# Performance work log

Hardware: AMD Instinct MI355X
Metric: run time of the kernel (lower is better)

The kernel has to match this reference:

```python
import jax, jax.numpy as jnp
import numpy as np

N_NODES = 100_000
N_FACES = 200_000
N_EDGES1 = 800_000
N_TRIP = 500_000
H = 64
GEO_IN = 10 + 2 * 23  # 56
N_INTER = 3
DEPTH = 3  # finaldepth; total SPNN layers = DEPTH + 1
PI = float(np.pi)
EPS = 1e-5


def setup_inputs() -> dict:
    key = jax.random.key(0)
    ks = jax.random.split(key, 12)
    s = 0.05
    input_feature = jax.random.normal(ks[0], (N_NODES, H), jnp.float32)
    coords = jax.random.normal(ks[1], (N_NODES, 3), jnp.float32)
    face_norm = jax.random.normal(ks[2], (N_FACES, 3), jnp.float32)
    face_x = jax.random.normal(ks[3], (N_FACES, 23), jnp.float32)
    edge_whichface = jax.random.randint(ks[4], (N_EDGES1,), 0, N_FACES)
    edge_index_2rd = jax.random.randint(ks[5], (3, N_TRIP), 0, N_NODES)
    edx_ij = jax.random.randint(ks[6], (N_TRIP,), 0, N_EDGES1)
    edx_rand = jax.random.randint(ks[7], (N_TRIP,), 0, N_EDGES1)
    edx_jk = jnp.where(jnp.arange(N_TRIP) % 2 == 0, edx_ij, edx_rand)
    att = jnp.ones((2,), jnp.float32)
    W_geo = jax.random.normal(ks[8], (H, GEO_IN), jnp.float32) * s
    b_geo = jnp.zeros((H,), jnp.float32)
    g_geo = jnp.ones((H,), jnp.float32)
    be_geo = jnp.zeros((H,), jnp.float32)
    spnn_W0 = jax.random.normal(ks[9], (N_INTER, 2, H, 4 * H), jnp.float32) * s
    spnn_b0 = jnp.zeros((N_INTER, 2, H), jnp.float32)
    spnn_Wr = jax.random.normal(ks[10], (N_INTER, 2, DEPTH, H, H), jnp.float32) * s
    spnn_br = jnp.zeros((N_INTER, 2, DEPTH, H), jnp.float32)
    bn_g = jnp.ones((N_INTER, 2, DEPTH + 1, H), jnp.float32)
    bn_b = jnp.zeros((N_INTER, 2, DEPTH + 1, H), jnp.float32)
    return dict(input_feature=input_feature, coords=coords, face_norm=face_norm,
                face_x=face_x, att=att, W_geo=W_geo, b_geo=b_geo, g_geo=g_geo,
                be_geo=be_geo, spnn_W0=spnn_W0, spnn_b0=spnn_b0, spnn_Wr=spnn_Wr,
                spnn_br=spnn_br, bn_g=bn_g, bn_b=bn_b,
                edge_whichface=edge_whichface, edge_index_2rd=edge_index_2rd,
                edx_jk=edx_jk, edx_ij=edx_ij)


def _bn(x, g, b):
    # BatchNorm1d, training mode (batch stats, biased variance)
    mean = x.mean(0)
    var = ((x - mean) ** 2).mean(0)
    return (x - mean) * jax.lax.rsqrt(var + EPS) * g + b


def _masked_bn(x, mf, g, b):
    # BatchNorm over only the masked rows (original code runs BN on x_i[mask]);
    # applied to all rows, masked rows selected afterward -> identical math.
    cnt = jnp.maximum(mf.sum(), 1.0)
    mean = (x * mf).sum(0) / cnt
    var = (((x - mean) ** 2) * mf).sum(0) / cnt
    return (x - mean) * jax.lax.rsqrt(var + EPS) * g + b


def _angle(v1, v2):
    c = jnp.cross(v1, v2)
    return jnp.arctan2(jnp.linalg.norm(c, axis=1), (v1 * v2).sum(1))


def reference(input_feature, coords, face_norm, face_x, att, W_geo, b_geo,
              g_geo, be_geo, spnn_W0, spnn_b0, spnn_Wr, spnn_br, bn_g, bn_b,
              edge_whichface, edge_index_2rd, edx_jk, edx_ij):
    i, j, k = edge_index_2rd
    f_ij = edge_whichface[edx_ij]
    f_jk = edge_whichface[edx_jk]
    # angle_face is computed then multiplied by 0 in the original
    angle_face = (PI - _angle(face_norm[f_ij], face_norm[f_jk])) * 0.0
    cj, ci, ck = coords[j], coords[i], coords[k]
    d_ij = jnp.linalg.norm(cj - ci, axis=1)
    d_jk = jnp.linalg.norm(cj - ck, axis=1)
    theta = _angle(cj - ci, ck - cj)
    same_face = f_ij == f_jk
    geo = jnp.concatenate([d_ij[:, None], d_jk[:, None], theta[:, None],
                           angle_face[:, None], cj, ci,
                           face_x[f_ij], face_x[f_jk]], axis=-1)  # [E, 56]
    geo = jax.nn.relu(_bn(geo @ W_geo.T + b_geo, g_geo, be_geo))  # [E, H]

    nf = input_feature
    masks = [same_face, ~same_face]
    outs = []
    for t in range(N_INTER):
        xcat = jnp.concatenate([nf[i], nf[j], nf[k], geo], axis=-1)  # [E, 4H]
        x_out = jnp.zeros((xcat.shape[0], H), xcat.dtype)
        for bi in range(2):
            mf = masks[bi].astype(xcat.dtype)[:, None]
            x = jax.nn.relu(_masked_bn(xcat @ spnn_W0[t, bi].T + spnn_b0[t, bi],
                                       mf, bn_g[t, bi, 0], bn_b[t, bi, 0]))
            for l in range(DEPTH):
                x = jax.nn.relu(_masked_bn(x @ spnn_Wr[t, bi, l].T + spnn_br[t, bi, l],
                                           mf, bn_g[t, bi, l + 1], bn_b[t, bi, l + 1]))
            x = jax.nn.leaky_relu(x) * att[bi]
            x_out = x_out + x * mf
        nf = jax.ops.segment_sum(x_out, i, num_segments=N_NODES)
        outs.append(nf)
    return jnp.stack(outs)  # [N_INTER, N, H] (list in original)
```

## Files before the change

kernel.cpp:

```cpp
#include <hip/hip_runtime.h>

#define E_TRIP 500000
#define EPAD   500224
#define NTILE64 (EPAD/64)
#define NBLK256 (EPAD/256)
#define NBLK    1954
#define NN 100000
#define NBIN (2*NN)
#define EPSF 1e-5f
#define RSTAT 64

typedef _Float16 f16;
typedef _Float16 f16x8 __attribute__((ext_vector_type(8)));
typedef float f32x4 __attribute__((ext_vector_type(4)));

__global__ __launch_bounds__(256) void k_count(const int* __restrict__ ewf,
    const int* __restrict__ exij, const int* __restrict__ exjk,
    unsigned char* __restrict__ biedge, int* __restrict__ cb0)
{
  __shared__ int wcnt[4];
  int e = blockIdx.x*256 + threadIdx.x;
  bool active = e < E_TRIP;
  int b = 0;
  if (active) {
    int fij = ewf[exij[e]];
    int fjk = ewf[exjk[e]];
    b = (fij == fjk) ? 0 : 1;
    biedge[e] = (unsigned char)b;
  }
  unsigned long long m0 = __ballot(active && b==0);
  int lane = threadIdx.x & 63, wv = threadIdx.x >> 6;
  if (lane == 0) wcnt[wv] = (int)__popcll(m0);
  __syncthreads();
  if (threadIdx.x == 0) cb0[blockIdx.x] = wcnt[0] + wcnt[1] + wcnt[2] + wcnt[3];
}

__global__ __launch_bounds__(1024) void k_scanb(const int* __restrict__ cb0, int* __restrict__ sc)
{
  __shared__ int s[2048];
  int tid = threadIdx.x;
  int i0 = tid, i1 = tid + 1024;
  s[i0] = (i0 < NBLK) ? cb0[i0] : 0;
  s[i1] = (i1 < NBLK) ? cb0[i1] : 0;
  __syncthreads();
  for (int off = 1; off < 2048; off <<= 1) {
    int v0 = (i0 >= off) ? s[i0 - off] : 0;
    int v1 = (i1 >= off) ? s[i1 - off] : 0;
    __syncthreads();
    s[i0] += v0; s[i1] += v1;
    __syncthreads();
  }
  if (tid == 0) {
    int c0 = s[NBLK-1];
    int c0p = (c0 + 63) & ~63;
    sc[4] = c0; sc[5] = c0p; sc[6] = E_TRIP - c0;
  }
}

__global__ __launch_bounds__(256) void k_cvt(const float* __restrict__ W0,
    const float* __restrict__ Wr, const float* __restrict__ nf,
    f16* __restrict__ W0h, f16* __restrict__ Wrh, f16* __restrict__ nfh)
{
  int i = (blockIdx.x*256 + threadIdx.x) * 4;
  if (i < 98304) {
    float4 v = *(const float4*)(W0 + i);
    W0h[i]=(f16)v.x; W0h[i+1]=(f16)v.y; W0h[i+2]=(f16)v.z; W0h[i+3]=(f16)v.w;
  } else if (i < 172032) {
    int j = i - 98304;
    float4 v = *(const float4*)(Wr + j);
    Wrh[j]=(f16)v.x; Wrh[j+1]=(f16)v.y; Wrh[j+2]=(f16)v.z; Wrh[j+3]=(f16)v.w;
  } else {
    int j = i - 172032;
    if (j < NN*64) {
      float4 v = *(const float4*)(nf + j);
      nfh[j]=(f16)v.x; nfh[j+1]=(f16)v.y; nfh[j+2]=(f16)v.z; nfh[j+3]=(f16)v.w;
    }
  }
}

__global__ __launch_bounds__(256) void k_hist(const unsigned char* __restrict__ biedge,
    const int* __restrict__ eidx, int* __restrict__ cnt)
{
  int e = blockIdx.x*256 + threadIdx.x;
  if (e < E_TRIP) {
    int key = (int)biedge[e]*NN + eidx[e];
    atomicAdd(&cnt[key], 1);
  }
}

__global__ __launch_bounds__(512) void k_scan1(const int* __restrict__ cnt,
    int* __restrict__ start, int* __restrict__ btot)
{
  __shared__ int s[512];
  int tid = threadIdx.x;
  int g = blockIdx.x*512 + tid;
  int x = (g < NBIN) ? cnt[g] : 0;
  s[tid] = x; __syncthreads();
  #pragma unroll
  for (int off = 1; off < 512; off <<= 1) {
    int v = (tid >= off) ? s[tid-off] : 0;
    __syncthreads();
    s[tid] += v;
    __syncthreads();
  }
  if (g < NBIN) start[g] = s[tid] - x;
  if (tid == 511) btot[blockIdx.x] = s[511];
}

__global__ __launch_bounds__(512) void k_scan2(int* __restrict__ btot)
{
  __shared__ int s[512];
  int tid = threadIdx.x;
  int x = (tid < 391) ? btot[tid] : 0;
  s[tid] = x; __syncthreads();
  #pragma unroll
  for (int off = 1; off < 512; off <<= 1) {
    int v = (tid >= off) ? s[tid-off] : 0;
    __syncthreads();
    s[tid] += v;
    __syncthreads();
  }
  if (tid < 391) btot[tid] = s[tid] - x;
}

__global__ __launch_bounds__(512) void k_scan3(int* __restrict__ start,
    int* __restrict__ cur, const int* __restrict__ btot, const int* __restrict__ sc)
{
  int tid = threadIdx.x;
  int g = blockIdx.x*512 + tid;
  if (g < NBIN) {
    int v = start[g] + btot[blockIdx.x];
    if (g >= NN) v += sc[5] - sc[4];
    start[g] = v;
    cur[g] = v;
  }
  if (g == 0) start[NBIN] = sc[5] + sc[6];
}

__global__ __launch_bounds__(256) void k_place(const unsigned char* __restrict__ biedge,
    const int* __restrict__ eidx, int* __restrict__ cur,
    int* __restrict__ epos, int* __restrict__ ip, int* __restrict__ jp, int* __restrict__ kp)
{
  int e = blockIdx.x*256 + threadIdx.x;
  if (e < E_TRIP) {
    int i = eidx[e];
    int key = (int)biedge[e]*NN + i;
    int pos = atomicAdd(&cur[key], 1);
    epos[pos] = e;
    ip[pos] = i;
    jp[pos] = eidx[E_TRIP + e];
    kp[pos] = eidx[2*E_TRIP + e];
  }
}

__global__ __launch_bounds__(256) void k_geo(
    const float* __restrict__ coords, const float* __restrict__ facex,
    const int* __restrict__ ewf, const int* __restrict__ exij, const int* __restrict__ exjk,
    const float* __restrict__ Wgeo, const float* __restrict__ bgeo,
    const int* __restrict__ sc, const int* __restrict__ epos,
    const int* __restrict__ ip, const int* __restrict__ jp, const int* __restrict__ kp,
    f16* __restrict__ zgeo, float* __restrict__ gstats)
{
  __shared__ f16 lds[256*72];
  __shared__ float sstat[64][2];
  int tid = threadIdx.x;
  int base = blockIdx.x*256;
  int c0 = sc[4], c0p = sc[5], c1 = sc[6];
  if (tid < 128) ((float*)sstat)[tid] = 0.f;
  {
    int p = base + tid;
    bool valid = (p < c0) || (p >= c0p && p < c0p + c1);
    f16* lrow = lds + tid*72;
    if (valid) {
      int e = epos[p];
      int ii = ip[p], jj = jp[p], kk = kp[p];
      float cix = coords[ii*3+0], ciy = coords[ii*3+1], ciz = coords[ii*3+2];
      float cjx = coords[jj*3+0], cjy = coords[jj*3+1], cjz = coords[jj*3+2];
      float ckx = coords[kk*3+0], cky = coords[kk*3+1], ckz = coords[kk*3+2];
      float v1x = cjx-cix, v1y = cjy-ciy, v1z = cjz-ciz;
      float v2x = ckx-cjx, v2y = cky-cjy, v2z = ckz-cjz;
      float dij = sqrtf(v1x*v1x + v1y*v1y + v1z*v1z);
      float djk = sqrtf(v2x*v2x + v2y*v2y + v2z*v2z);
      float cx = v1y*v2z - v1z*v2y;
      float cy = v1z*v2x - v1x*v2z;
      float cz = v1x*v2y - v1y*v2x;
      float theta = atan2f(sqrtf(cx*cx+cy*cy+cz*cz), v1x*v2x+v1y*v2y+v1z*v2z);
      lrow[0]=(f16)dij; lrow[1]=(f16)djk; lrow[2]=(f16)theta; lrow[3]=(f16)0.f;
      lrow[4]=(f16)cjx; lrow[5]=(f16)cjy; lrow[6]=(f16)cjz;
      lrow[7]=(f16)cix; lrow[8]=(f16)ciy; lrow[9]=(f16)ciz;
      int fij = ewf[exij[e]], fjk = ewf[exjk[e]];
      const float* fx1 = facex + (size_t)fij*23;
      const float* fx2 = facex + (size_t)fjk*23;
      for (int c = 0; c < 23; c++) lrow[10+c] = (f16)fx1[c];
      for (int c = 0; c < 23; c++) lrow[33+c] = (f16)fx2[c];
      for (int c = 56; c < 64; c++) lrow[c] = (f16)0.f;
    } else {
      for (int c = 0; c < 64; c++) lrow[c] = (f16)0.f;
    }
  }
  __syncthreads();
  int wv = tid>>6, lane = tid&63, lg = lane>>4, lr = lane&15;
  f16x8 Bf[4][2];
  #pragma unroll
  for (int nt = 0; nt < 4; nt++) {
    #pragma unroll
    for (int ks = 0; ks < 2; ks++) {
      int n = nt*16 + lr;
      int kb = ks*32 + lg*8;
      f16x8 w;
      if (kb < 56) {
        float4 w0 = *(const float4*)(Wgeo + n*56 + kb);
        float4 w1 = *(const float4*)(Wgeo + n*56 + kb + 4);
        w[0]=(f16)w0.x; w[1]=(f16)w0.y; w[2]=(f16)w0.z; w[3]=(f16)w0.w;
        w[4]=(f16)w1.x; w[5]=(f16)w1.y; w[6]=(f16)w1.z; w[7]=(f16)w1.w;
      } else {
        #pragma unroll
        for (int j2 = 0; j2 < 8; j2++) w[j2] = (f16)0.f;
      }
      Bf[nt][ks] = w;
    }
  }
  float ssum[4] = {0,0,0,0}, ssq[4] = {0,0,0,0};
  for (int mt = 0; mt < 4; mt++) {
    int rbase = wv*64 + mt*16;
    f16x8 A0 = *(const f16x8*)(lds + (rbase+lr)*72 + lg*8);
    f16x8 A1 = *(const f16x8*)(lds + (rbase+lr)*72 + 32 + lg*8);
    f32x4 acc[4];
    #pragma unroll
    for (int nt = 0; nt < 4; nt++) { acc[nt][0]=0.f; acc[nt][1]=0.f; acc[nt][2]=0.f; acc[nt][3]=0.f; }
    #pragma unroll
    for (int nt = 0; nt < 4; nt++) {
      acc[nt] = __builtin_amdgcn_mfma_f32_16x16x32_f16(A0, Bf[nt][0], acc[nt], 0, 0, 0);
      acc[nt] = __builtin_amdgcn_mfma_f32_16x16x32_f16(A1, Bf[nt][1], acc[nt], 0, 0, 0);
    }
    #pragma unroll
    for (int nt = 0; nt < 4; nt++) {
      int n = nt*16 + lr;
      float bg = bgeo[n];
      #pragma unroll
      for (int rg = 0; rg < 4; rg++) {
        int rloc = rbase + lg*4 + rg;
        int p = base + rloc;
        bool valid = (p < c0) || (p >= c0p && p < c0p + c1);
        float z = valid ? (acc[nt][rg] + bg) : 0.f;
        ssum[nt] += z; ssq[nt] += z*z;
        lds[rloc*72 + n] = (f16)z;
      }
    }
  }
  #pragma unroll
  for (int nt = 0; nt < 4; nt++) {
    float v = ssum[nt]; v += __shfl_xor(v, 16); v += __shfl_xor(v, 32);
    float w = ssq[nt];  w += __shfl_xor(w, 16); w += __shfl_xor(w, 32);
    if (lane < 16) { atomicAdd(&sstat[nt*16+lane][0], v); atomicAdd(&sstat[nt*16+lane][1], w); }
  }
  __syncthreads();
  {
    int p = base + tid;
    #pragma unroll
    for (int c = 0; c < 8; c++) {
      f16x8 v = *(const f16x8*)(lds + tid*72 + c*8);
      *(f16x8*)(zgeo + (size_t)p*64 + c*8) = v;
    }
  }
  if (tid < 128) {
    float v = ((float*)sstat)[tid];
    if (v != 0.f) atomicAdd(&gstats[(blockIdx.x & (RSTAT-1))*256 + tid], v);
  }
}

__global__ __launch_bounds__(256) void k_layer0(
    const f16* __restrict__ nfsrc, const f16* __restrict__ zgeo,
    const f16* __restrict__ W0p, const float* __restrict__ b0p,
    const float* __restrict__ g_geo, const float* __restrict__ be_geo,
    const float* __restrict__ geostats, float* __restrict__ outstats,
    const int* __restrict__ sc, const int* __restrict__ ip,
    const int* __restrict__ jp, const int* __restrict__ kp,
    f16* __restrict__ z0)
{
  __shared__ f16 lds[64*264];
  __shared__ float geoscale[64], geoshift[64];
  __shared__ float sstat[2][64][2];
  int tid = threadIdx.x;
  int c0 = sc[4], c0p = sc[5], c1 = sc[6];
  if (tid < 64) {
    float s = 0.f, sq = 0.f;
    #pragma unroll 8
    for (int r = 0; r < RSTAT; r++) {
      s  += geostats[r*256 + tid*2];
      sq += geostats[r*256 + tid*2 + 1];
    }
    float mean = s * (1.f/(float)E_TRIP);
    float var  = sq * (1.f/(float)E_TRIP) - mean*mean;
    float rstd = rsqrtf(var + EPSF);
    float scl = g_geo[tid]*rstd;
    geoscale[tid] = scl;
    geoshift[tid] = be_geo[tid] - mean*scl;
  }
  ((float*)sstat)[tid] = 0.f;
  __syncthreads();
  int wv = tid>>6, lane = tid&63, lg = lane>>4, lr = lane&15;
  float s0sum[4]={0,0,0,0}, s0sq[4]={0,0,0,0}, s1sum[4]={0,0,0,0}, s1sq[4]={0,0,0,0};
  for (int tile = blockIdx.x; tile < NTILE64; tile += gridDim.x) {
    int rowbase = tile*64;
    int branch = (rowbase >= c0p) ? 1 : 0;
    {
      int r = tid >> 2, q = tid & 3;
      int p = rowbase + r;
      bool valid = (p < c0) || (p >= c0p && p < c0p + c1);
      f16* rowp = lds + r*264 + q*64;
      if (q < 3) {
        if (valid) {
          int idx = (q==0 ? ip : (q==1 ? jp : kp))[p];
          const f16* src = nfsrc + (size_t)idx*64;
          #pragma unroll
          for (int c = 0; c < 8; c++) *(f16x8*)(rowp + c*8) = *(const f16x8*)(src + c*8);
        } else {
          f16x8 u;
          #pragma unroll
          for (int j2 = 0; j2 < 8; j2++) u[j2] = (f16)0.f;
          #pragma unroll
          for (int c = 0; c < 8; c++) *(f16x8*)(rowp + c*8) = u;
        }
      } else {
        if (valid) {
          const f16* zg = zgeo + (size_t)p*64;
          #pragma unroll
          for (int c = 0; c < 8; c++) {
            f16x8 raw = *(const f16x8*)(zg + c*8);
            f16x8 u;
            #pragma unroll
            for (int j2 = 0; j2 < 8; j2++) {
              int f = c*8 + j2;
              float x = fmaxf((float)raw[j2]*geoscale[f] + geoshift[f], 0.f);
              u[j2] = (f16)x;
            }
            *(f16x8*)(rowp + c*8) = u;
          }
        } else {
          f16x8 u;
          #pragma unroll
          for (int j2 = 0; j2 < 8; j2++) u[j2] = (f16)0.f;
          #pragma unroll
          for (int c = 0; c < 8; c++) *(f16x8*)(rowp + c*8) = u;
        }
      }
    }
    __syncthreads();
    {
      int r0 = wv*16;
      const f16* Wb = W0p + branch*16384;
      f32x4 acc[4];
      #pragma unroll
      for (int nt = 0; nt < 4; nt++) { acc[nt][0]=0.f; acc[nt][1]=0.f; acc[nt][2]=0.f; acc[nt][3]=0.f; }
      #pragma unroll
      for (int ks = 0; ks < 8; ks++) {
        f16x8 A = *(const f16x8*)(lds + (r0+lr)*264 + (ks*4+lg)*8);
        #pragma unroll
        for (int nt = 0; nt < 4; nt++) {
          f16x8 B = *(const f16x8*)(Wb + (nt*16+lr)*256 + ks*32 + lg*8);
          acc[nt] = __builtin_amdgcn_mfma_f32_16x16x32_f16(A, B, acc[nt], 0, 0, 0);
        }
      }
      #pragma unroll
      for (int nt = 0; nt < 4; nt++) {
        int n = nt*16 + lr;
        float bias = b0p[branch*64 + n];
        #pragma unroll
        for (int rg = 0; rg < 4; rg++) {
          int rloc = r0 + lg*4 + rg;
          int p = rowbase + rloc;
          bool valid = (p < c0) || (p >= c0p && p < c0p + c1);
          float z = valid ? (acc[nt][rg] + bias) : 0.f;
          if (branch == 0) { s0sum[nt] += z; s0sq[nt] += z*z; }
          else             { s1sum[nt] += z; s1sq[nt] += z*z; }
          lds[rloc*264 + n] = (f16)z;
        }
      }
    }
    __syncthreads();
    {
      int r = tid>>2, q = tid&3;
      int p = rowbase + r;
      f16x8 v0 = *(const f16x8*)(lds + r*264 + q*16);
      f16x8 v1 = *(const f16x8*)(lds + r*264 + q*16 + 8);
      *(f16x8*)(z0 + (size_t)p*64 + q*16) = v0;
      *(f16x8*)(z0 + (size_t)p*64 + q*16 + 8) = v1;
    }
    __syncthreads();
  }
  #pragma unroll
  for (int nt = 0; nt < 4; nt++) {
    float v, w;
    v = s0sum[nt]; v += __shfl_xor(v,16); v += __shfl_xor(v,32);
    w = s0sq[nt];  w += __shfl_xor(w,16); w += __shfl_xor(w,32);
    if (lane < 16) { atomicAdd(&sstat[0][nt*16+lane][0], v); atomicAdd(&sstat[0][nt*16+lane][1], w); }
    v = s1sum[nt]; v += __shfl_xor(v,16); v += __shfl_xor(v,32);
    w = s1sq[nt];  w += __shfl_xor(w,16); w += __shfl_xor(w,32);
    if (lane < 16) { atomicAdd(&sstat[1][nt*16+lane][0], v); atomicAdd(&sstat[1][nt*16+lane][1], w); }
  }
  __syncthreads();
  {
    float v = ((float*)sstat)[tid];
    if (v != 0.f) atomicAdd(&outstats[(blockIdx.x & (RSTAT-1))*256 + tid], v);
  }
}

__global__ __launch_bounds__(256) void k_hidden(
    const f16* __restrict__ zin, f16* __restrict__ zout,
    const f16* __restrict__ Wp, const float* __restrict__ biasp,
    const float* __restrict__ bngp, const float* __restrict__ bnbp,
    const float* __restrict__ instats, float* __restrict__ outstats,
    const int* __restrict__ sc)
{
  __shared__ float lscale[2][64], lshift[2][64];
  __shared__ float sstat[2][64][2];
  __shared__ f16 ldso[4][16*72];
  int tid = threadIdx.x;
  int c0 = sc[4], c0p = sc[5], c1 = sc[6];
  if (tid < 128) {
    int b = tid>>6, n = tid&63;
    int cb = b ? c1 : c0; if (cb < 1) cb = 1;
    float inv = 1.f/(float)cb;
    int idx = (b*64+n)*2;
    float s = 0.f, sq = 0.f;
    #pragma unroll 8
    for (int r = 0; r < RSTAT; r++) {
      s  += instats[r*256 + idx];
      sq += instats[r*256 + idx + 1];
    }
    float mean = s*inv, var = sq*inv - mean*mean;
    float rstd = rsqrtf(var + EPSF);
    float scl = bngp[b*256+n]*rstd;
    lscale[b][n] = scl;
    lshift[b][n] = bnbp[b*256+n] - mean*scl;
  }
  ((float*)sstat)[tid] = 0.f;
  __syncthreads();
  int wv = tid>>6, lane = tid&63, lg = lane>>4, lr = lane&15;
  f16* myldso = ldso[wv];
  float s0sum[4]={0,0,0,0}, s0sq[4]={0,0,0,0}, s1sum[4]={0,0,0,0}, s1sq[4]={0,0,0,0};
  for (int tile = blockIdx.x; tile < NTILE64; tile += gridDim.x) {
    int rowbase = tile*64;
    int branch = (rowbase >= c0p) ? 1 : 0;
    int rgl = rowbase + wv*16 + lr;
    f16x8 Af[2];
    #pragma unroll
    for (int ks = 0; ks < 2; ks++) {
      f16x8 raw = *(const f16x8*)(zin + (size_t)rgl*64 + ks*32 + lg*8);
      f16x8 A;
      #pragma unroll
      for (int j2 = 0; j2 < 8; j2++) {
        int f = ks*32 + lg*8 + j2;
        float x = fmaxf((float)raw[j2]*lscale[branch][f] + lshift[branch][f], 0.f);
        A[j2] = (f16)x;
      }
      Af[ks] = A;
    }
    f32x4 acc[4];
    #pragma unroll
    for (int nt = 0; nt < 4; nt++) { acc[nt][0]=0.f; acc[nt][1]=0.f; acc[nt][2]=0.f; acc[nt][3]=0.f; }
    #pragma unroll
    for (int ks = 0; ks < 2; ks++) {
      #pragma unroll
      for (int nt = 0; nt < 4; nt++) {
        f16x8 B = *(const f16x8*)(Wp + branch*12288 + (nt*16+lr)*64 + ks*32 + lg*8);
        acc[nt] = __builtin_amdgcn_mfma_f32_16x16x32_f16(Af[ks], B, acc[nt], 0, 0, 0);
      }
    }
    #pragma unroll
    for (int nt = 0; nt < 4; nt++) {
      int n = nt*16 + lr;
      float bias = biasp[branch*192 + n];
      #pragma unroll
      for (int rg = 0; rg < 4; rg++) {
        int rloc = lg*4 + rg;
        int p = rowbase + wv*16 + rloc;
        bool valid = (p < c0) || (p >= c0p && p < c0p + c1);
        float z = valid ? (acc[nt][rg] + bias) : 0.f;
        if (branch == 0) { s0sum[nt] += z; s0sq[nt] += z*z; }
        else             { s1sum[nt] += z; s1sq[nt] += z*z; }
        myldso[rloc*72 + n] = (f16)z;
      }
    }
    {
      int r2 = lane>>2, q = lane&3;
      int p2 = rowbase + wv*16 + r2;
      f16x8 v0 = *(const f16x8*)(myldso + r2*72 + q*8);
      f16x8 v1 = *(const f16x8*)(myldso + r2*72 + 32 + q*8);
      *(f16x8*)(zout + (size_t)p2*64 + q*8) = v0;
      *(f16x8*)(zout + (size_t)p2*64 + 32 + q*8) = v1;
    }
  }
  #pragma unroll
  for (int nt = 0; nt < 4; nt++) {
    float v, w;
    v = s0sum[nt]; v += __shfl_xor(v,16); v += __shfl_xor(v,32);
    w = s0sq[nt];  w += __shfl_xor(w,16); w += __shfl_xor(w,32);
    if (lane < 16) { atomicAdd(&sstat[0][nt*16+lane][0], v); atomicAdd(&sstat[0][nt*16+lane][1], w); }
    v = s1sum[nt]; v += __shfl_xor(v,16); v += __shfl_xor(v,32);
    w = s1sq[nt];  w += __shfl_xor(w,16); w += __shfl_xor(w,32);
    if (lane < 16) { atomicAdd(&sstat[1][nt*16+lane][0], v); atomicAdd(&sstat[1][nt*16+lane][1], w); }
  }
  __syncthreads();
  {
    float v = ((float*)sstat)[tid];
    if (v != 0.f) atomicAdd(&outstats[(blockIdx.x & (RSTAT-1))*256 + tid], v);
  }
}

__global__ __launch_bounds__(256) void k_scatter(
    const f16* __restrict__ z3, const float* __restrict__ att,
    const float* __restrict__ bngp, const float* __restrict__ bnbp,
    const float* __restrict__ instats, const int* __restrict__ sc,
    const int* __restrict__ astart,
    float* __restrict__ outt, f16* __restrict__ nfh)
{
  __shared__ float lscale[2][64], lshift[2][64];
  int tid = threadIdx.x;
  int c0 = sc[4];
  {
    int c0p = sc[5], c1 = sc[6];
    (void)c0p; (void)c1;
    if (tid < 128) {
      int b = tid>>6, n = tid&63;
      int cb = b ? sc[6] : sc[4]; if (cb < 1) cb = 1;
      float inv = 1.f/(float)cb;
      int idx = (b*64+n)*2;
      float s = 0.f, sq = 0.f;
      #pragma unroll 8
      for (int r = 0; r < RSTAT; r++) {
        s  += instats[r*256 + idx];
        sq += instats[r*256 + idx + 1];
      }
      float mean = s*inv, var = sq*inv - mean*mean;
      float rstd = rsqrtf(var + EPSF);
      float scl = bngp[b*256+n]*rstd;
      lscale[b][n] = scl;
      lshift[b][n] = bnbp[b*256+n] - mean*scl;
    }
  }
  __syncthreads();
  int gid = blockIdx.x*256 + tid;
  int n = gid >> 3, q = gid & 7;
  if (n >= NN) return;
  int s0 = astart[n];
  int e0 = astart[n+1]; if (e0 > c0) e0 = c0;
  int s1 = astart[NN+n];
  int e1 = astart[NN+n+1];
  float a0 = att[0], a1 = att[1];
  float acc[8] = {0,0,0,0,0,0,0,0};
  float scb[8], shb[8];
  #pragma unroll
  for (int j2 = 0; j2 < 8; j2++) { scb[j2] = lscale[0][q*8+j2]; shb[j2] = lshift[0][q*8+j2]; }
  for (int t = s0; t < e0; t++) {
    f16x8 raw = *(const f16x8*)(z3 + (size_t)t*64 + q*8);
    #pragma unroll
    for (int j2 = 0; j2 < 8; j2++) {
      float x = (float)raw[j2]*scb[j2] + shb[j2];
      acc[j2] += fmaxf(x, 0.f) * a0;
    }
  }
  #pragma unroll
  for (int j2 = 0; j2 < 8; j2++) { scb[j2] = lscale[1][q*8+j2]; shb[j2] = lshift[1][q*8+j2]; }
  for (int t = s1; t < e1; t++) {
    f16x8 raw = *(const f16x8*)(z3 + (size_t)t*64 + q*8);
    #pragma unroll
    for (int j2 = 0; j2 < 8; j2++) {
      float x = (float)raw[j2]*scb[j2] + shb[j2];
      acc[j2] += fmaxf(x, 0.f) * a1;
    }
  }
  float4 lo, hi;
  lo.x=acc[0]; lo.y=acc[1]; lo.z=acc[2]; lo.w=acc[3];
  hi.x=acc[4]; hi.y=acc[5]; hi.z=acc[6]; hi.w=acc[7];
  *(float4*)(outt + (size_t)n*64 + q*8) = lo;
  *(float4*)(outt + (size_t)n*64 + q*8 + 4) = hi;
  f16x8 h;
  #pragma unroll
  for (int j2 = 0; j2 < 8; j2++) h[j2] = (f16)acc[j2];
  *(f16x8*)(nfh + (size_t)n*64 + q*8) = h;
}

extern "C" void kernel_launch(void* const* d_in, const int* in_sizes, int n_in,
                              void* d_out, int out_size, void* d_ws, size_t ws_size,
                              hipStream_t stream)
{
  const float* input_feature = (const float*)d_in[0];
  const float* coords   = (const float*)d_in[1];
  const float* face_x   = (const float*)d_in[3];
  const float* att      = (const float*)d_in[4];
  const float* W_geo    = (const float*)d_in[5];
  const float* b_geo    = (const float*)d_in[6];
  const float* g_geo    = (const float*)d_in[7];
  const float* be_geo   = (const float*)d_in[8];
  const float* spnn_W0  = (const float*)d_in[9];
  const float* spnn_b0  = (const float*)d_in[10];
  const float* spnn_Wr  = (const float*)d_in[11];
  const float* spnn_br  = (const float*)d_in[12];
  const float* bn_g     = (const float*)d_in[13];
  const float* bn_b     = (const float*)d_in[14];
  const int* ewf  = (const int*)d_in[15];
  const int* eidx = (const int*)d_in[16];
  const int* exjk = (const int*)d_in[17];
  const int* exij = (const int*)d_in[18];
  float* out = (float*)d_out;
  char* ws = (char*)d_ws;

  size_t off = 0;
  auto take = [&](size_t bytes) -> char* {
    size_t o = off; off = (off + bytes + 255) & ~(size_t)255; return ws + o;
  };
  const size_t STATBUF = (size_t)RSTAT*256;
  int*   sc     = (int*)take(256);
  float* stats  = (float*)take(13*STATBUF*sizeof(float));
  int*   cb0    = (int*)take(sizeof(int)*2048);
  int*   cnt    = (int*)take(sizeof(int)*NBIN);
  int*   astart = (int*)take(sizeof(int)*(NBIN+1));
  int*   curn   = (int*)take(sizeof(int)*NBIN);
  int*   btot   = (int*)take(sizeof(int)*512);
  unsigned char* biedge = (unsigned char*)take(E_TRIP);
  int* epos = (int*)take(sizeof(int)*EPAD);
  int* ip   = (int*)take(sizeof(int)*EPAD);
  int* jp   = (int*)take(sizeof(int)*EPAD);
  int* kp   = (int*)take(sizeof(int)*EPAD);
  f16* W0h  = (f16*)take(sizeof(f16)*3*2*64*256);
  f16* Wrh  = (f16*)take(sizeof(f16)*3*2*3*64*64);
  f16* nf16 = (f16*)take(sizeof(f16)*(size_t)NN*64);
  f16* zgeo = (f16*)take(sizeof(f16)*(size_t)EPAD*64);
  f16* zA   = (f16*)take(sizeof(f16)*(size_t)EPAD*64);
  f16* zB   = (f16*)take(sizeof(f16)*(size_t)EPAD*64);
  if (off > ws_size) return;

  hipMemsetAsync(sc, 0, 256, stream);
  hipMemsetAsync(stats, 0, 13*STATBUF*sizeof(float), stream);
  hipMemsetAsync(cnt, 0, sizeof(int)*NBIN, stream);

  k_count <<<NBLK, 256, 0, stream>>>(ewf, exij, exjk, biedge, cb0);
  k_scanb <<<1, 1024, 0, stream>>>(cb0, sc);
  k_cvt   <<<6418, 256, 0, stream>>>(spnn_W0, spnn_Wr, input_feature, W0h, Wrh, nf16);
  k_hist  <<<NBLK, 256, 0, stream>>>(biedge, eidx, cnt);
  k_scan1 <<<391, 512, 0, stream>>>(cnt, astart, btot);
  k_scan2 <<<1, 512, 0, stream>>>(btot);
  k_scan3 <<<391, 512, 0, stream>>>(astart, curn, btot, sc);
  k_place <<<NBLK, 256, 0, stream>>>(biedge, eidx, curn, epos, ip, jp, kp);

  k_geo   <<<NBLK256, 256, 0, stream>>>(coords, face_x, ewf, exij, exjk, W_geo, b_geo,
                                        sc, epos, ip, jp, kp, zgeo, stats);
  for (int t = 0; t < 3; t++) {
    float* outt = out + (size_t)t*NN*64;
    k_layer0<<<1024, 256, 0, stream>>>(nf16, zgeo,
        W0h + (size_t)t*2*64*256, spnn_b0 + t*2*64,
        g_geo, be_geo, stats, stats + (size_t)(1 + t*4)*STATBUF,
        sc, ip, jp, kp, zA);
    f16* zi = zA; f16* zo = zB;
    for (int h = 0; h < 3; h++) {
      k_hidden<<<2048, 256, 0, stream>>>(zi, zo,
          Wrh + (size_t)t*2*3*64*64 + (size_t)h*64*64,
          spnn_br + t*2*3*64 + h*64,
          bn_g + t*2*4*64 + h*64,
          bn_b + t*2*4*64 + h*64,
          stats + (size_t)(1 + t*4 + h)*STATBUF,
          stats + (size_t)(1 + t*4 + h + 1)*STATBUF,
          sc);
      f16* tmp = zi; zi = zo; zo = tmp;
    }
    k_scatter<<<(NN*8 + 255)/256, 256, 0, stream>>>(zi, att,
        bn_g + t*2*4*64 + 3*64, bn_b + t*2*4*64 + 3*64,
        stats + (size_t)(1 + t*4 + 3)*STATBUF, sc, astart, outt, nf16);
  }
}
```

Before: 1.386 ms.

## Hoist geo batchnorm into one pass and feed geo operand directly to MFMA

Adds a kernel that applies geo BatchNorm+ReLU in place once after k_geo, instead of recomputing it inside each of the three layer-0 launches. Layer-0 now loads the normalized geo slice straight from global memory into MFMA operand registers, shrinking the LDS tile from 264 to 200 halfs per row. Grid sizes for layer0 and hidden kernels are changed to 1954 blocks. The trade-off is one extra read/write pass over the geo buffer, and invalid rows no longer have their geo input zeroed, although their outputs are still masked.

Measured after the change: 1.416 ms. +2.2%, slower.

```diff
diff --git a/kernel.cpp b/kernel.cpp
--- a/kernel.cpp
+++ b/kernel.cpp
@@ -269,34 +269,52 @@
   }
 }
 
-__global__ __launch_bounds__(256) void k_layer0(
-    const f16* __restrict__ nfsrc, const f16* __restrict__ zgeo,
-    const f16* __restrict__ W0p, const float* __restrict__ b0p,
+__global__ __launch_bounds__(256) void k_geobn(f16* __restrict__ zg,
     const float* __restrict__ g_geo, const float* __restrict__ be_geo,
-    const float* __restrict__ geostats, float* __restrict__ outstats,
-    const int* __restrict__ sc, const int* __restrict__ ip,
-    const int* __restrict__ jp, const int* __restrict__ kp,
-    f16* __restrict__ z0)
-{
-  __shared__ f16 lds[64*264];
-  __shared__ float geoscale[64], geoshift[64];
-  __shared__ float sstat[2][64][2];
-  int tid = threadIdx.x;
-  int c0 = sc[4], c0p = sc[5], c1 = sc[6];
+    const float* __restrict__ gstats)
+{
+  __shared__ float scale[64], shift[64];
+  int tid = threadIdx.x;
   if (tid < 64) {
     float s = 0.f, sq = 0.f;
     #pragma unroll 8
     for (int r = 0; r < RSTAT; r++) {
-      s  += geostats[r*256 + tid*2];
-      sq += geostats[r*256 + tid*2 + 1];
+      s  += gstats[r*256 + tid*2];
+      sq += gstats[r*256 + tid*2 + 1];
     }
     float mean = s * (1.f/(float)E_TRIP);
     float var  = sq * (1.f/(float)E_TRIP) - mean*mean;
     float rstd = rsqrtf(var + EPSF);
     float scl = g_geo[tid]*rstd;
-    geoscale[tid] = scl;
-    geoshift[tid] = be_geo[tid] - mean*scl;
-  }
+    scale[tid] = scl;
+    shift[tid] = be_geo[tid] - mean*scl;
+  }
+  __syncthreads();
+  size_t idx = ((size_t)blockIdx.x*256 + tid) * 8;
+  if (idx >= (size_t)EPAD*64) return;
+  int f0 = (int)(idx & 63);
+  f16x8 raw = *(const f16x8*)(zg + idx);
+  f16x8 u;
+  #pragma unroll
+  for (int j2 = 0; j2 < 8; j2++) {
+    float x = fmaxf((float)raw[j2]*scale[f0+j2] + shift[f0+j2], 0.f);
+    u[j2] = (f16)x;
+  }
+  *(f16x8*)(zg + idx) = u;
+}
+
+__global__ __launch_bounds__(256) void k_layer0(
+    const f16* __restrict__ nfsrc, const f16* __restrict__ zgbn,
+    const f16* __restrict__ W0p, const float* __restrict__ b0p,
+    float* __restrict__ outstats,
+    const int* __restrict__ sc, const int* __restrict__ ip,
+    const int* __restrict__ jp, const int* __restrict__ kp,
+    f16* __restrict__ z0)
+{
+  __shared__ f16 lds[64*200];
+  __shared__ float sstat[2][64][2];
+  int tid = threadIdx.x;
+  int c0 = sc[4], c0p = sc[5], c1 = sc[6];
   ((float*)sstat)[tid] = 0.f;
   __syncthreads();
   int wv = tid>>6, lane = tid&63, lg = lane>>4, lr = lane&15;
@@ -304,12 +322,15 @@
   for (int tile = blockIdx.x; tile < NTILE64; tile += gridDim.x) {
     int rowbase = tile*64;
     int branch = (rowbase >= c0p) ? 1 : 0;
+    int pr = rowbase + wv*16 + lr;
+    f16x8 G0 = *(const f16x8*)(zgbn + (size_t)pr*64 + lg*8);
+    f16x8 G1 = *(const f16x8*)(zgbn + (size_t)pr*64 + 32 + lg*8);
     {
       int r = tid >> 2, q = tid & 3;
-      int p = rowbase + r;
-      bool valid = (p < c0) || (p >= c0p && p < c0p + c1);
-      f16* rowp = lds + r*264 + q*64;
       if (q < 3) {
+        int p = rowbase + r;
+        bool valid = (p < c0) || (p >= c0p && p < c0p + c1);
+        f16* rowp = lds + r*200 + q*64;
         if (valid) {
           int idx = (q==0 ? ip : (q==1 ? jp : kp))[p];
           const f16* src = nfsrc + (size_t)idx*64;
@@ -322,28 +343,6 @@
           #pragma unroll
           for (int c = 0; c < 8; c++) *(f16x8*)(rowp + c*8) = u;
         }
-      } else {
-        if (valid) {
-          const f16* zg = zgeo + (size_t)p*64;
-          #pragma unroll
-          for (int c = 0; c < 8; c++) {
-            f16x8 raw = *(const f16x8*)(zg + c*8);
-            f16x8 u;
-            #pragma unroll
-            for (int j2 = 0; j2 < 8; j2++) {
-              int f = c*8 + j2;
-              float x = fmaxf((float)raw[j2]*geoscale[f] + geoshift[f], 0.f);
-              u[j2] = (f16)x;
-            }
-            *(f16x8*)(rowp + c*8) = u;
-          }
-        } else {
-          f16x8 u;
-          #pragma unroll
-          for (int j2 = 0; j2 < 8; j2++) u[j2] = (f16)0.f;
-          #pragma unroll
-          for (int c = 0; c < 8; c++) *(f16x8*)(rowp + c*8) = u;
-        }
       }
     }
     __syncthreads();
@@ -354,14 +353,22 @@
       #pragma unroll
       for (int nt = 0; nt < 4; nt++) { acc[nt][0]=0.f; acc[nt][1]=0.f; acc[nt][2]=0.f; acc[nt][3]=0.f; }
       #pragma unroll
-      for (int ks = 0; ks < 8; ks++) {
-        f16x8 A = *(const f16x8*)(lds + (r0+lr)*264 + (ks*4+lg)*8);
+      for (int ks = 0; ks < 6; ks++) {
+        f16x8 A = *(const f16x8*)(lds + (r0+lr)*200 + ks*32 + lg*8);
         #pragma unroll
         for (int nt = 0; nt < 4; nt++) {
           f16x8 B = *(const f16x8*)(Wb + (nt*16+lr)*256 + ks*32 + lg*8);
           acc[nt] = __builtin_amdgcn_mfma_f32_16x16x32_f16(A, B, acc[nt], 0, 0, 0);
         }
       }
+      #pragma unroll
+      for (int nt = 0; nt < 4; nt++) {
+        f16x8 B0 = *(const f16x8*)(Wb + (nt*16+lr)*256 + 192 + lg*8);
+        acc[nt] = __builtin_amdgcn_mfma_f32_16x16x32_f16(G0, B0, acc[nt], 0, 0, 0);
+        f16x8 B1 = *(const f16x8*)(Wb + (nt*16+lr)*256 + 224 + lg*8);
+        acc[nt] = __builtin_amdgcn_mfma_f32_16x16x32_f16(G1, B1, acc[nt], 0, 0, 0);
+      }
+      __syncthreads();
       #pragma unroll
       for (int nt = 0; nt < 4; nt++) {
         int n = nt*16 + lr;
@@ -374,7 +381,7 @@
           float z = valid ? (acc[nt][rg] + bias) : 0.f;
           if (branch == 0) { s0sum[nt] += z; s0sq[nt] += z*z; }
           else             { s1sum[nt] += z; s1sq[nt] += z*z; }
-          lds[rloc*264 + n] = (f16)z;
+          lds[rloc*200 + n] = (f16)z;
         }
       }
     }
@@ -382,8 +389,8 @@
     {
       int r = tid>>2, q = tid&3;
       int p = rowbase + r;
-      f16x8 v0 = *(const f16x8*)(lds + r*264 + q*16);
-      f16x8 v1 = *(const f16x8*)(lds + r*264 + q*16 + 8);
+      f16x8 v0 = *(const f16x8*)(lds + r*200 + q*16);
+      f16x8 v1 = *(const f16x8*)(lds + r*200 + q*16 + 8);
       *(f16x8*)(z0 + (size_t)p*64 + q*16) = v0;
       *(f16x8*)(z0 + (size_t)p*64 + q*16 + 8) = v1;
     }
@@ -520,8 +527,6 @@
   int tid = threadIdx.x;
   int c0 = sc[4];
   {
-    int c0p = sc[5], c1 = sc[6];
-    (void)c0p; (void)c1;
     if (tid < 128) {
       int b = tid>>6, n = tid&63;
       int cb = b ? sc[6] : sc[4]; if (cb < 1) cb = 1;
@@ -647,15 +652,16 @@
 
   k_geo   <<<NBLK256, 256, 0, stream>>>(coords, face_x, ewf, exij, exjk, W_geo, b_geo,
                                         sc, epos, ip, jp, kp, zgeo, stats);
+  k_geobn <<<(EPAD*64/8 + 255)/256, 256, 0, stream>>>(zgeo, g_geo, be_geo, stats);
   for (int t = 0; t < 3; t++) {
     float* outt = out + (size_t)t*NN*64;
-    k_layer0<<<1024, 256, 0, stream>>>(nf16, zgeo,
+    k_layer0<<<1954, 256, 0, stream>>>(nf16, zgeo,
         W0h + (size_t)t*2*64*256, spnn_b0 + t*2*64,
-        g_geo, be_geo, stats, stats + (size_t)(1 + t*4)*STATBUF,
+        stats + (size_t)(1 + t*4)*STATBUF,
         sc, ip, jp, kp, zA);
     f16* zi = zA; f16* zo = zB;
     for (int h = 0; h < 3; h++) {
-      k_hidden<<<2048, 256, 0, stream>>>(zi, zo,
+      k_hidden<<<1954, 256, 0, stream>>>(zi, zo,
           Wrh + (size_t)t*2*3*64*64 + (size_t)h*64*64,
           spnn_br + t*2*3*64 + h*64,
           bn_g + t*2*4*64 + h*64,
```
